# Kernel tuning notes

Hardware: AMD Instinct MI355X
Metric: run time of the kernel (lower is better)

## Reference

```python
import jax, jax.numpy as jnp
import numpy as np

N = 500_000        # atoms
P = 16_000_000     # neighbor pairs (half list)
NS = 4             # species types
CUTOFF = 2.5
BOX = 20.0         # cubic box edge length


def setup_inputs() -> dict:
    key = jax.random.key(0)
    k = jax.random.split(key, 6)
    positions = jax.random.uniform(k[0], (N, 3), dtype=jnp.float32) * BOX
    cell = jnp.eye(3, dtype=jnp.float32) * BOX
    pair_i = jax.random.randint(k[1], (P,), 0, N, dtype=jnp.int32)
    # guarantee j != i so r2 > 0 even when shift == 0
    offs = jax.random.randint(k[2], (P,), 1, N, dtype=jnp.int32)
    pair_j = (pair_i + offs) % N
    shifts = jax.random.randint(k[3], (P, 3), 0, 3, dtype=jnp.int32)
    species = jax.random.randint(k[4], (N,), 0, NS, dtype=jnp.int32)
    # per-species-pair LJ parameter tables (symmetric), mirroring the
    # dict {(a,b): (sigma, epsilon)} precomputation in __init__
    sig = 0.8 + 0.1 * jnp.arange(NS, dtype=jnp.float32)
    eps = 0.5 + 0.1 * jnp.arange(NS, dtype=jnp.float32)
    sigma_tab = 0.5 * (sig[:, None] + sig[None, :])
    eps_tab = jnp.sqrt(eps[:, None] * eps[None, :])
    sr = sigma_tab / CUTOFF
    shift_tab = 4.0 * eps_tab * (sr ** 12 - sr ** 6)
    return dict(positions=positions, cell=cell, sigma_tab=sigma_tab,
                eps_tab=eps_tab, shift_tab=shift_tab, species=species,
                pair_i=pair_i, pair_j=pair_j, shifts=shifts)


def reference(positions, cell, sigma_tab, eps_tab, shift_tab,
              species, pair_i, pair_j, shifts):
    # gather species-pair params (vectorized dict lookup)
    si = species[pair_i]
    sj = species[pair_j]
    sigma = sigma_tab[si, sj]        # [P]
    epsilon = eps_tab[si, sj]        # [P]
    shift_e = shift_tab[si, sj]      # [P]
    # displacement with periodic cell shift: r_j - r_i + S @ cell
    d = positions[pair_j] - positions[pair_i] + shifts.astype(positions.dtype) @ cell  # [P,3]
    r2 = jnp.sum(d * d, axis=-1)     # [P]
    r6 = r2 * r2 * r2
    sigma3 = sigma * sigma * sigma
    sigma6 = sigma3 * sigma3
    sr6 = sigma6 / r6
    sr12 = sr6 * sr6
    e = 4.0 * epsilon * (sr12 - sr6) - shift_e   # [P]
    # per-atom energy: half to each endpoint (per_atom=True path)
    energy = jnp.zeros(positions.shape[0], dtype=positions.dtype)
    energy = energy.at[pair_i].add(0.5 * e).at[pair_j].add(0.5 * e)
    return energy
```

## Files before the change

kernel.cpp:

```cpp
#include <hip/hip_runtime.h>


#define BUCKET_SHIFT 11
#define BUCKET_SIZE  2048
#define SLICES       8
#define QSCALE       2048.0f
#define QINV         (1.0f / 2048.0f)

__global__ void lj_zero_kernel(float* __restrict__ out, long n) {
    long i = (long)blockIdx.x * blockDim.x + threadIdx.x;
    if (i < n) out[i] = 0.0f;
}

__global__ void lj_pack8_kernel(const float* __restrict__ pos,
                                const int* __restrict__ species,
                                unsigned long long* __restrict__ tab8,
                                int* __restrict__ cursor,
                                int nb, int cap, int n) {
    int i = blockIdx.x * blockDim.x + threadIdx.x;
    if (i < n) {
        unsigned int ux = (unsigned int)(pos[3 * i]     * QSCALE + 0.5f) & 0xFFFFu;
        unsigned int uy = (unsigned int)(pos[3 * i + 1] * QSCALE + 0.5f) & 0xFFFFu;
        unsigned int uz = (unsigned int)(pos[3 * i + 2] * QSCALE + 0.5f) & 0xFFFFu;
        unsigned long long w = (unsigned long long)ux
                             | ((unsigned long long)uy << 16)
                             | ((unsigned long long)uz << 32)
                             | ((unsigned long long)(species[i] & 3) << 48);
        tab8[i] = w;
    }
    if (i < nb) cursor[i] = i * cap;
}

__global__ void lj_pack_kernel(const float* __restrict__ pos,
                               const int* __restrict__ species,
                               float4* __restrict__ packed, int n) {
    int i = blockIdx.x * blockDim.x + threadIdx.x;
    if (i < n) {
        float4 p;
        p.x = pos[3 * i];
        p.y = pos[3 * i + 1];
        p.z = pos[3 * i + 2];
        p.w = __int_as_float(species[i]);
        packed[i] = p;
    }
}

__device__ __forceinline__ unsigned int lj_encode(float he) {
    unsigned int u = __float_as_uint(he);
    return (u + 0x400u) & 0xFFFFF800u;
}

__global__ __launch_bounds__(1024) void lj_passA_kernel(
    const unsigned long long* __restrict__ tab8,
    const float* __restrict__ cell,
    const float* __restrict__ sigma_tab,
    const float* __restrict__ eps_tab,
    const float* __restrict__ shift_tab,
    const int* __restrict__ pair_i,
    const int* __restrict__ pair_j,
    const int* __restrict__ shifts,
    unsigned int* __restrict__ record_buf,
    int* __restrict__ cursor,
    int cap, int nb, int P)
{
    __shared__ float s_sig6[16];
    __shared__ float s_eps4[16];
    __shared__ float s_shift[16];
    __shared__ float s_cell[9];
    __shared__ int hist[256];
    __shared__ int basev[256];
    __shared__ int bbase[256];
    __shared__ unsigned int staged[8192];
    __shared__ unsigned char bucketOf[8192];
    int t = threadIdx.x;
    if (t < 16) {
        float s = sigma_tab[t];
        float s3 = s * s * s;
        s_sig6[t] = s3 * s3;
        s_eps4[t] = 4.0f * eps_tab[t];
        s_shift[t] = shift_tab[t];
    }
    if (t < 9) s_cell[t] = cell[t];
    if (t < 256) hist[t] = 0;
    __syncthreads();

    float c00 = s_cell[0], c01 = s_cell[1], c02 = s_cell[2];
    float c10 = s_cell[3], c11 = s_cell[4], c12 = s_cell[5];
    float c20 = s_cell[6], c21 = s_cell[7], c22 = s_cell[8];

    long base = (long)(blockIdx.x * (long)blockDim.x + t) * 4;

    int   ai[4], aj[4];
    float hev[4];
    int   sloti[4], slotj[4];
    bool  valid[4];

    if (base + 3 < P) {
        int4 pi4 = *(const int4*)(pair_i + base);
        int4 pj4 = *(const int4*)(pair_j + base);
        int4 sA = *(const int4*)(shifts + base * 3);
        int4 sB = *(const int4*)(shifts + base * 3 + 4);
        int4 sC = *(const int4*)(shifts + base * 3 + 8);
        int pis[4] = {pi4.x, pi4.y, pi4.z, pi4.w};
        int pjs[4] = {pj4.x, pj4.y, pj4.z, pj4.w};
        int shv[12] = {sA.x, sA.y, sA.z, sA.w, sB.x, sB.y, sB.z, sB.w,
                       sC.x, sC.y, sC.z, sC.w};
#pragma unroll
        for (int k = 0; k < 4; ++k) {
            int i = pis[k], j = pjs[k];
            float fx = (float)shv[3 * k], fy = (float)shv[3 * k + 1], fz = (float)shv[3 * k + 2];
            unsigned long long gi = tab8[i];
            unsigned long long gj = tab8[j];
            int xi = (int)(gi & 0xFFFFu), yi = (int)((gi >> 16) & 0xFFFFu), zi = (int)((gi >> 32) & 0xFFFFu);
            int xj = (int)(gj & 0xFFFFu), yj = (int)((gj >> 16) & 0xFFFFu), zj = (int)((gj >> 32) & 0xFFFFu);
            float dlx = (float)(xj - xi) * QINV;
            float dly = (float)(yj - yi) * QINV;
            float dlz = (float)(zj - zi) * QINV;
            float dx = dlx + fx * c00 + fy * c10 + fz * c20;
            float dy = dly + fx * c01 + fy * c11 + fz * c21;
            float dz = dlz + fx * c02 + fy * c12 + fz * c22;
            float r2 = dx * dx + dy * dy + dz * dz;
            float r6 = r2 * r2 * r2;
            int idx = (int)(gi >> 48) * 4 + (int)(gj >> 48);
            float sr6 = s_sig6[idx] / r6;
            float sr12 = sr6 * sr6;
            hev[k] = 0.5f * (s_eps4[idx] * (sr12 - sr6) - s_shift[idx]);
            ai[k] = i; aj[k] = j; valid[k] = true;
        }
    } else {
#pragma unroll
        for (int k = 0; k < 4; ++k) {
            long p = base + k;
            valid[k] = (p < P);
            ai[k] = 0; aj[k] = 0; hev[k] = 0.0f;
            if (valid[k]) {
                int i = pair_i[p], j = pair_j[p];
                float fx = (float)shifts[3 * p], fy = (float)shifts[3 * p + 1], fz = (float)shifts[3 * p + 2];
                unsigned long long gi = tab8[i];
                unsigned long long gj = tab8[j];
                int xi = (int)(gi & 0xFFFFu), yi = (int)((gi >> 16) & 0xFFFFu), zi = (int)((gi >> 32) & 0xFFFFu);
                int xj = (int)(gj & 0xFFFFu), yj = (int)((gj >> 16) & 0xFFFFu), zj = (int)((gj >> 32) & 0xFFFFu);
                float dlx = (float)(xj - xi) * QINV;
                float dly = (float)(yj - yi) * QINV;
                float dlz = (float)(zj - zi) * QINV;
                float dx = dlx + fx * c00 + fy * c10 + fz * c20;
                float dy = dly + fx * c01 + fy * c11 + fz * c21;
                float dz = dlz + fx * c02 + fy * c12 + fz * c22;
                float r2 = dx * dx + dy * dy + dz * dz;
                float r6 = r2 * r2 * r2;
                int idx = (int)(gi >> 48) * 4 + (int)(gj >> 48);
                float sr6 = s_sig6[idx] / r6;
                float sr12 = sr6 * sr6;
                hev[k] = 0.5f * (s_eps4[idx] * (sr12 - sr6) - s_shift[idx]);
                ai[k] = i; aj[k] = j;
            }
        }
    }

#pragma unroll
    for (int k = 0; k < 4; ++k) {
        if (valid[k]) {
            sloti[k] = atomicAdd(&hist[ai[k] >> BUCKET_SHIFT], 1);
            slotj[k] = atomicAdd(&hist[aj[k] >> BUCKET_SHIFT], 1);
        } else {
            sloti[k] = 0; slotj[k] = 0;
        }
    }
    __syncthreads();

    if (t < 64) {
        int b0 = t * 4;
        int h0 = hist[b0], h1 = hist[b0 + 1], h2 = hist[b0 + 2], h3 = hist[b0 + 3];
        int s = h0 + h1 + h2 + h3;
        int incl = s;
#pragma unroll
        for (int d = 1; d < 64; d <<= 1) {
            int v = __shfl_up(incl, d, 64);
            if (t >= d) incl += v;
        }
        int excl = incl - s;
        bbase[b0]     = excl;
        bbase[b0 + 1] = excl + h0;
        bbase[b0 + 2] = excl + h0 + h1;
        bbase[b0 + 3] = excl + h0 + h1 + h2;
    }
    if (t < nb) {
        int h = hist[t];
        basev[t] = (h > 0) ? atomicAdd(&cursor[t], h) : 0;
    }
    __syncthreads();

#pragma unroll
    for (int k = 0; k < 4; ++k) {
        if (valid[k]) {
            unsigned int u = lj_encode(hev[k]);
            int bi = ai[k] >> BUCKET_SHIFT;
            int li = bbase[bi] + sloti[k];
            staged[li] = u | (unsigned int)(ai[k] & (BUCKET_SIZE - 1));
            bucketOf[li] = (unsigned char)bi;
            int bj = aj[k] >> BUCKET_SHIFT;
            int lidxj = bbase[bj] + slotj[k];
            staged[lidxj] = u | (unsigned int)(aj[k] & (BUCKET_SIZE - 1));
            bucketOf[lidxj] = (unsigned char)bj;
        }
    }
    __syncthreads();

    int total = bbase[255] + hist[255];
    for (int idx = t; idx < total; idx += 1024) {
        int b = (int)bucketOf[idx];
        int g = basev[b] + (idx - bbase[b]);
        if (g < (b + 1) * cap) record_buf[g] = staged[idx];
    }
}

__global__ __launch_bounds__(256) void lj_passB_kernel(
    const unsigned int* __restrict__ record_buf,
    const int* __restrict__ cursor,
    float* __restrict__ partial,
    int cap)
{
    __shared__ float e[BUCKET_SIZE];
    int blk = blockIdx.x;
    int b = blk >> 3;
    int s = blk & (SLICES - 1);
    int t = threadIdx.x;
#pragma unroll
    for (int k = 0; k < 8; ++k) e[t + 256 * k] = 0.0f;
    __syncthreads();

    int begin = b * cap;
    int count = cursor[b] - begin;
    if (count > cap) count = cap;

    int ngroups = (count + 7) >> 3;
    int gps = (ngroups + SLICES - 1) / SLICES;
    int g0 = s * gps;
    int g1 = g0 + gps;
    if (g1 > ngroups) g1 = ngroups;

    for (int g = g0 + t; g < g1; g += 256) {
        int r0 = g * 8;
        const unsigned int* rp = record_buf + begin + r0;
        if (r0 + 8 <= count) {
            int4 a = *(const int4*)(rp);
            int4 c = *(const int4*)(rp + 4);
            unsigned int w0 = (unsigned int)a.x, w1 = (unsigned int)a.y;
            unsigned int w2 = (unsigned int)a.z, w3 = (unsigned int)a.w;
            unsigned int w4 = (unsigned int)c.x, w5 = (unsigned int)c.y;
            unsigned int w6 = (unsigned int)c.z, w7 = (unsigned int)c.w;
            atomicAdd(&e[w0 & 2047u], __uint_as_float(w0 & 0xFFFFF800u));
            atomicAdd(&e[w1 & 2047u], __uint_as_float(w1 & 0xFFFFF800u));
            atomicAdd(&e[w2 & 2047u], __uint_as_float(w2 & 0xFFFFF800u));
            atomicAdd(&e[w3 & 2047u], __uint_as_float(w3 & 0xFFFFF800u));
            atomicAdd(&e[w4 & 2047u], __uint_as_float(w4 & 0xFFFFF800u));
            atomicAdd(&e[w5 & 2047u], __uint_as_float(w5 & 0xFFFFF800u));
            atomicAdd(&e[w6 & 2047u], __uint_as_float(w6 & 0xFFFFF800u));
            atomicAdd(&e[w7 & 2047u], __uint_as_float(w7 & 0xFFFFF800u));
        } else {
            for (int r = r0; r < count; ++r) {
                unsigned int w = record_buf[begin + r];
                atomicAdd(&e[w & 2047u], __uint_as_float(w & 0xFFFFF800u));
            }
        }
    }
    __syncthreads();

    float* pb = partial + (long)blk * BUCKET_SIZE;
#pragma unroll
    for (int k = 0; k < 8; ++k) pb[t + 256 * k] = e[t + 256 * k];
}

__global__ void lj_reduce_kernel(const float* __restrict__ partial,
                                 float* __restrict__ energy, int N) {
    int i = blockIdx.x * blockDim.x + threadIdx.x;
    if (i < N) {
        int b = i >> BUCKET_SHIFT;
        int l = i & (BUCKET_SIZE - 1);
        const float* pb = partial + ((long)b * SLICES) * BUCKET_SIZE + l;
        float s = 0.0f;
#pragma unroll
        for (int k = 0; k < SLICES; ++k) s += pb[(long)k * BUCKET_SIZE];
        energy[i] = s;
    }
}

__device__ __forceinline__ void lj_one_pair_packed(
    int i, int j, float fx, float fy, float fz,
    const float4* __restrict__ packed,
    const float* s_sig6, const float* s_eps4, const float* s_shift,
    float c00, float c01, float c02,
    float c10, float c11, float c12,
    float c20, float c21, float c22,
    float* __restrict__ energy)
{
    float4 gi = packed[i];
    float4 gj = packed[j];
    float dx = gj.x - gi.x + fx * c00 + fy * c10 + fz * c20;
    float dy = gj.y - gi.y + fx * c01 + fy * c11 + fz * c21;
    float dz = gj.z - gi.z + fx * c02 + fy * c12 + fz * c22;
    float r2 = dx * dx + dy * dy + dz * dz;
    float r6 = r2 * r2 * r2;
    int idx = __float_as_int(gi.w) * 4 + __float_as_int(gj.w);
    float sr6 = s_sig6[idx] / r6;
    float sr12 = sr6 * sr6;
    float he = 0.5f * (s_eps4[idx] * (sr12 - sr6) - s_shift[idx]);
    atomicAdd(energy + i, he);
    atomicAdd(energy + j, he);
}

__global__ __launch_bounds__(256) void lj_pairs_packed_kernel(
    const float4* __restrict__ packed,
    const float* __restrict__ cell,
    const float* __restrict__ sigma_tab,
    const float* __restrict__ eps_tab,
    const float* __restrict__ shift_tab,
    const int* __restrict__ pair_i,
    const int* __restrict__ pair_j,
    const int* __restrict__ shifts,
    float* __restrict__ energy,
    int P)
{
    __shared__ float s_sig6[16];
    __shared__ float s_eps4[16];
    __shared__ float s_shift[16];
    __shared__ float s_cell[9];
    int t = threadIdx.x;
    if (t < 16) {
        float s = sigma_tab[t];
        float s3 = s * s * s;
        s_sig6[t] = s3 * s3;
        s_eps4[t] = 4.0f * eps_tab[t];
        s_shift[t] = shift_tab[t];
    }
    if (t < 9) s_cell[t] = cell[t];
    __syncthreads();

    float c00 = s_cell[0], c01 = s_cell[1], c02 = s_cell[2];
    float c10 = s_cell[3], c11 = s_cell[4], c12 = s_cell[5];
    float c20 = s_cell[6], c21 = s_cell[7], c22 = s_cell[8];

    long base = (long)(blockIdx.x * (long)blockDim.x + t) * 4;
    if (base + 3 < P) {
        int4 pi4 = *(const int4*)(pair_i + base);
        int4 pj4 = *(const int4*)(pair_j + base);
        int4 sA = *(const int4*)(shifts + base * 3);
        int4 sB = *(const int4*)(shifts + base * 3 + 4);
        int4 sC = *(const int4*)(shifts + base * 3 + 8);
        int pis[4] = {pi4.x, pi4.y, pi4.z, pi4.w};
        int pjs[4] = {pj4.x, pj4.y, pj4.z, pj4.w};
        int shv[12] = {sA.x, sA.y, sA.z, sA.w, sB.x, sB.y, sB.z, sB.w,
                       sC.x, sC.y, sC.z, sC.w};
#pragma unroll
        for (int k = 0; k < 4; ++k) {
            lj_one_pair_packed(pis[k], pjs[k],
                        (float)shv[3 * k], (float)shv[3 * k + 1], (float)shv[3 * k + 2],
                        packed, s_sig6, s_eps4, s_shift,
                        c00, c01, c02, c10, c11, c12, c20, c21, c22, energy);
        }
    } else {
        for (long p = base; p < P; ++p) {
            lj_one_pair_packed(pair_i[p], pair_j[p],
                        (float)shifts[3 * p], (float)shifts[3 * p + 1], (float)shifts[3 * p + 2],
                        packed, s_sig6, s_eps4, s_shift,
                        c00, c01, c02, c10, c11, c12, c20, c21, c22, energy);
        }
    }
}

__device__ __forceinline__ void lj_one_pair(
    int i, int j, float fx, float fy, float fz,
    const float* __restrict__ pos,
    const int* __restrict__ species,
    const float* s_sig6, const float* s_eps4, const float* s_shift,
    float c00, float c01, float c02,
    float c10, float c11, float c12,
    float c20, float c21, float c22,
    float* __restrict__ energy)
{
    float dx = pos[3 * j]     - pos[3 * i]     + fx * c00 + fy * c10 + fz * c20;
    float dy = pos[3 * j + 1] - pos[3 * i + 1] + fx * c01 + fy * c11 + fz * c21;
    float dz = pos[3 * j + 2] - pos[3 * i + 2] + fx * c02 + fy * c12 + fz * c22;
    float r2 = dx * dx + dy * dy + dz * dz;
    float r6 = r2 * r2 * r2;
    int idx = species[i] * 4 + species[j];
    float sr6 = s_sig6[idx] / r6;
    float sr12 = sr6 * sr6;
    float he = 0.5f * (s_eps4[idx] * (sr12 - sr6) - s_shift[idx]);
    atomicAdd(energy + i, he);
    atomicAdd(energy + j, he);
}

__global__ __launch_bounds__(256) void lj_pairs_kernel(
    const float* __restrict__ pos,
    const float* __restrict__ cell,
    const float* __restrict__ sigma_tab,
    const float* __restrict__ eps_tab,
    const float* __restrict__ shift_tab,
    const int* __restrict__ species,
    const int* __restrict__ pair_i,
    const int* __restrict__ pair_j,
    const int* __restrict__ shifts,
    float* __restrict__ energy,
    int P)
{
    __shared__ float s_sig6[16];
    __shared__ float s_eps4[16];
    __shared__ float s_shift[16];
    __shared__ float s_cell[9];
    int t = threadIdx.x;
    if (t < 16) {
        float s = sigma_tab[t];
        float s3 = s * s * s;
        s_sig6[t] = s3 * s3;
        s_eps4[t] = 4.0f * eps_tab[t];
        s_shift[t] = shift_tab[t];
    }
    if (t < 9) s_cell[t] = cell[t];
    __syncthreads();

    float c00 = s_cell[0], c01 = s_cell[1], c02 = s_cell[2];
    float c10 = s_cell[3], c11 = s_cell[4], c12 = s_cell[5];
    float c20 = s_cell[6], c21 = s_cell[7], c22 = s_cell[8];

    long base = (long)(blockIdx.x * (long)blockDim.x + t) * 4;
    if (base + 3 < P) {
        int4 pi4 = *(const int4*)(pair_i + base);
        int4 pj4 = *(const int4*)(pair_j + base);
        int4 sA = *(const int4*)(shifts + base * 3);
        int4 sB = *(const int4*)(shifts + base * 3 + 4);
        int4 sC = *(const int4*)(shifts + base * 3 + 8);
        int pis[4] = {pi4.x, pi4.y, pi4.z, pi4.w};
        int pjs[4] = {pj4.x, pj4.y, pj4.z, pj4.w};
        int shv[12] = {sA.x, sA.y, sA.z, sA.w, sB.x, sB.y, sB.z, sB.w,
                       sC.x, sC.y, sC.z, sC.w};
#pragma unroll
        for (int k = 0; k < 4; ++k) {
            lj_one_pair(pis[k], pjs[k],
                        (float)shv[3 * k], (float)shv[3 * k + 1], (float)shv[3 * k + 2],
                        pos, species, s_sig6, s_eps4, s_shift,
                        c00, c01, c02, c10, c11, c12, c20, c21, c22, energy);
        }
    } else {
        for (long p = base; p < P; ++p) {
            lj_one_pair(pair_i[p], pair_j[p],
                        (float)shifts[3 * p], (float)shifts[3 * p + 1], (float)shifts[3 * p + 2],
                        pos, species, s_sig6, s_eps4, s_shift,
                        c00, c01, c02, c10, c11, c12, c20, c21, c22, energy);
        }
    }
}

extern "C" void kernel_launch(void* const* d_in, const int* in_sizes, int n_in,
                              void* d_out, int out_size, void* d_ws, size_t ws_size,
                              hipStream_t stream) {
    const float* positions = (const float*)d_in[0];
    const float* cell      = (const float*)d_in[1];
    const float* sigma_tab = (const float*)d_in[2];
    const float* eps_tab   = (const float*)d_in[3];
    const float* shift_tab = (const float*)d_in[4];
    const int*   species   = (const int*)d_in[5];
    const int*   pair_i    = (const int*)d_in[6];
    const int*   pair_j    = (const int*)d_in[7];
    const int*   shifts    = (const int*)d_in[8];
    float* energy = (float*)d_out;

    const int N = out_size;
    const int P = in_sizes[6];

    const int threads = 256;
    const int ablocks = (N + threads - 1) / threads;
    const int pblocks4 = (int)((((long)P + 3) / 4 + threads - 1) / threads);

    const int nb = (N + BUCKET_SIZE - 1) / BUCKET_SIZE;
    long avg = (2L * P) / (nb > 0 ? nb : 1);
    long capl = (avg + avg / 50 + 512 + 1023) & ~1023L;
    const int cap = (int)capl;
    const size_t rec_bytes  = (size_t)nb * (size_t)cap * 4u;
    const size_t tab_bytes  = (size_t)N * 8u;
    const size_t cur_bytes  = (size_t)nb * 4u;
    const size_t part_bytes = (size_t)nb * SLICES * BUCKET_SIZE * 4u;
    const size_t need_bucket = rec_bytes + tab_bytes + cur_bytes + part_bytes;
    const size_t need_pack   = (size_t)N * 16u;

    const bool has_ws = (d_ws != nullptr);
    const bool sane = (nb > 0) && (nb <= 256) && ((long)nb * cap < 2000000000L);
    const bool use_bucket = has_ws && sane && (ws_size >= need_bucket);
    const bool use_pack   = has_ws && !use_bucket && (ws_size >= need_pack);

    if (use_bucket) {
        unsigned int* record_buf = (unsigned int*)d_ws;
        unsigned long long* tab8 = (unsigned long long*)((char*)d_ws + rec_bytes);
        int* cursor = (int*)((char*)d_ws + rec_bytes + tab_bytes);
        float* partial = (float*)((char*)d_ws + rec_bytes + tab_bytes + cur_bytes);

        lj_pack8_kernel<<<ablocks, threads, 0, stream>>>(
            positions, species, tab8, cursor, nb, cap, N);
        const int athreads = 1024;
        const long nthreads_needed = ((long)P + 3) / 4;
        const int pblocksA = (int)((nthreads_needed + athreads - 1) / athreads);
        lj_passA_kernel<<<pblocksA, athreads, 0, stream>>>(
            tab8, cell, sigma_tab, eps_tab, shift_tab,
            pair_i, pair_j, shifts, record_buf, cursor, cap, nb, P);
        lj_passB_kernel<<<nb * SLICES, threads, 0, stream>>>(record_buf, cursor, partial, cap);
        lj_reduce_kernel<<<ablocks, threads, 0, stream>>>(partial, energy, N);
    } else if (use_pack) {
        float4* packed = (float4*)d_ws;
        lj_zero_kernel<<<ablocks, threads, 0, stream>>>(energy, N);
        lj_pack_kernel<<<ablocks, threads, 0, stream>>>(positions, species, packed, N);
        lj_pairs_packed_kernel<<<pblocks4, threads, 0, stream>>>(
            packed, cell, sigma_tab, eps_tab, shift_tab,
            pair_i, pair_j, shifts, energy, P);
    } else {
        lj_zero_kernel<<<ablocks, threads, 0, stream>>>(energy, N);
        lj_pairs_kernel<<<pblocks4, threads, 0, stream>>>(
            positions, cell, sigma_tab, eps_tab, shift_tab, species,
            pair_i, pair_j, shifts, energy, P);
    }
}
```

Measured before the change: 752.6 us.

## Batch 8 pairs per thread in pass A with hoisted gathers and nontemporal streams

Pass A now handles 8 pairs per thread with 512-thread blocks, so each block still stages 8192 records. All 16 position-table gathers are issued before any arithmetic, which gives more memory-level parallelism. Pair indices, shifts and record output use nontemporal loads and stores so the streamed data does not pollute the cache. Records are encoded early and bucket/slot pairs are packed into single ints to save registers, though the higher per-thread register use may reduce occupancy.

```diff
diff --git a/kernel.cpp b/kernel.cpp
--- a/kernel.cpp
+++ b/kernel.cpp
@@ -6,6 +6,11 @@
 #define SLICES       8
 #define QSCALE       2048.0f
 #define QINV         (1.0f / 2048.0f)
+
+#define A_THREADS 512
+#define A_PAIRS   8
+
+typedef int vint4 __attribute__((ext_vector_type(4)));
 
 __global__ void lj_zero_kernel(float* __restrict__ out, long n) {
     long i = (long)blockIdx.x * blockDim.x + threadIdx.x;
@@ -50,7 +55,7 @@
     return (u + 0x400u) & 0xFFFFF800u;
 }
 
-__global__ __launch_bounds__(1024) void lj_passA_kernel(
+__global__ __launch_bounds__(A_THREADS) void lj_passA_kernel(
     const unsigned long long* __restrict__ tab8,
     const float* __restrict__ cell,
     const float* __restrict__ sigma_tab,
@@ -70,8 +75,8 @@
     __shared__ int hist[256];
     __shared__ int basev[256];
     __shared__ int bbase[256];
-    __shared__ unsigned int staged[8192];
-    __shared__ unsigned char bucketOf[8192];
+    __shared__ unsigned int staged[A_THREADS * A_PAIRS * 2];
+    __shared__ unsigned char bucketOf[A_THREADS * A_PAIRS * 2];
     int t = threadIdx.x;
     if (t < 16) {
         float s = sigma_tab[t];
@@ -88,31 +93,45 @@
     float c10 = s_cell[3], c11 = s_cell[4], c12 = s_cell[5];
     float c20 = s_cell[6], c21 = s_cell[7], c22 = s_cell[8];
 
-    long base = (long)(blockIdx.x * (long)blockDim.x + t) * 4;
-
-    int   ai[4], aj[4];
-    float hev[4];
-    int   sloti[4], slotj[4];
-    bool  valid[4];
-
-    if (base + 3 < P) {
-        int4 pi4 = *(const int4*)(pair_i + base);
-        int4 pj4 = *(const int4*)(pair_j + base);
-        int4 sA = *(const int4*)(shifts + base * 3);
-        int4 sB = *(const int4*)(shifts + base * 3 + 4);
-        int4 sC = *(const int4*)(shifts + base * 3 + 8);
-        int pis[4] = {pi4.x, pi4.y, pi4.z, pi4.w};
-        int pjs[4] = {pj4.x, pj4.y, pj4.z, pj4.w};
-        int shv[12] = {sA.x, sA.y, sA.z, sA.w, sB.x, sB.y, sB.z, sB.w,
-                       sC.x, sC.y, sC.z, sC.w};
-#pragma unroll
-        for (int k = 0; k < 4; ++k) {
-            int i = pis[k], j = pjs[k];
+    long base = (long)(blockIdx.x * (long)A_THREADS + t) * A_PAIRS;
+
+    unsigned int encI[A_PAIRS], encJ[A_PAIRS];
+    int slotij[A_PAIRS];
+    int bkt[A_PAIRS];
+    int vmask = 0;
+
+    if (base + (A_PAIRS - 1) < P) {
+        vmask = (1 << A_PAIRS) - 1;
+        vint4 piA = __builtin_nontemporal_load((const vint4*)(pair_i + base));
+        vint4 piB = __builtin_nontemporal_load((const vint4*)(pair_i + base + 4));
+        vint4 pjA = __builtin_nontemporal_load((const vint4*)(pair_j + base));
+        vint4 pjB = __builtin_nontemporal_load((const vint4*)(pair_j + base + 4));
+        int pis[A_PAIRS] = {piA[0], piA[1], piA[2], piA[3], piB[0], piB[1], piB[2], piB[3]};
+        int pjs[A_PAIRS] = {pjA[0], pjA[1], pjA[2], pjA[3], pjB[0], pjB[1], pjB[2], pjB[3]};
+
+        unsigned long long gi[A_PAIRS], gj[A_PAIRS];
+#pragma unroll
+        for (int k = 0; k < A_PAIRS; ++k) {
+            gi[k] = tab8[pis[k]];
+            gj[k] = tab8[pjs[k]];
+        }
+
+        vint4 s0 = __builtin_nontemporal_load((const vint4*)(shifts + base * 3));
+        vint4 s1 = __builtin_nontemporal_load((const vint4*)(shifts + base * 3 + 4));
+        vint4 s2 = __builtin_nontemporal_load((const vint4*)(shifts + base * 3 + 8));
+        vint4 s3 = __builtin_nontemporal_load((const vint4*)(shifts + base * 3 + 12));
+        vint4 s4 = __builtin_nontemporal_load((const vint4*)(shifts + base * 3 + 16));
+        vint4 s5 = __builtin_nontemporal_load((const vint4*)(shifts + base * 3 + 20));
+        int shv[24] = {s0[0], s0[1], s0[2], s0[3], s1[0], s1[1], s1[2], s1[3],
+                       s2[0], s2[1], s2[2], s2[3], s3[0], s3[1], s3[2], s3[3],
+                       s4[0], s4[1], s4[2], s4[3], s5[0], s5[1], s5[2], s5[3]};
+
+#pragma unroll
+        for (int k = 0; k < A_PAIRS; ++k) {
             float fx = (float)shv[3 * k], fy = (float)shv[3 * k + 1], fz = (float)shv[3 * k + 2];
-            unsigned long long gi = tab8[i];
-            unsigned long long gj = tab8[j];
-            int xi = (int)(gi & 0xFFFFu), yi = (int)((gi >> 16) & 0xFFFFu), zi = (int)((gi >> 32) & 0xFFFFu);
-            int xj = (int)(gj & 0xFFFFu), yj = (int)((gj >> 16) & 0xFFFFu), zj = (int)((gj >> 32) & 0xFFFFu);
+            unsigned long long wi = gi[k], wj = gj[k];
+            int xi = (int)(wi & 0xFFFFu), yi = (int)((wi >> 16) & 0xFFFFu), zi = (int)((wi >> 32) & 0xFFFFu);
+            int xj = (int)(wj & 0xFFFFu), yj = (int)((wj >> 16) & 0xFFFFu), zj = (int)((wj >> 32) & 0xFFFFu);
             float dlx = (float)(xj - xi) * QINV;
             float dly = (float)(yj - yi) * QINV;
             float dlz = (float)(zj - zi) * QINV;
@@ -121,25 +140,28 @@
             float dz = dlz + fx * c02 + fy * c12 + fz * c22;
             float r2 = dx * dx + dy * dy + dz * dz;
             float r6 = r2 * r2 * r2;
-            int idx = (int)(gi >> 48) * 4 + (int)(gj >> 48);
+            int idx = (int)(wi >> 48) * 4 + (int)(wj >> 48);
             float sr6 = s_sig6[idx] / r6;
             float sr12 = sr6 * sr6;
-            hev[k] = 0.5f * (s_eps4[idx] * (sr12 - sr6) - s_shift[idx]);
-            ai[k] = i; aj[k] = j; valid[k] = true;
+            float he = 0.5f * (s_eps4[idx] * (sr12 - sr6) - s_shift[idx]);
+            unsigned int u = lj_encode(he);
+            encI[k] = u | (unsigned int)(pis[k] & (BUCKET_SIZE - 1));
+            encJ[k] = u | (unsigned int)(pjs[k] & (BUCKET_SIZE - 1));
+            bkt[k] = (pis[k] >> BUCKET_SHIFT) | ((pjs[k] >> BUCKET_SHIFT) << 8);
         }
     } else {
 #pragma unroll
-        for (int k = 0; k < 4; ++k) {
+        for (int k = 0; k < A_PAIRS; ++k) {
             long p = base + k;
-            valid[k] = (p < P);
-            ai[k] = 0; aj[k] = 0; hev[k] = 0.0f;
-            if (valid[k]) {
+            encI[k] = 0; encJ[k] = 0; bkt[k] = 0;
+            if (p < P) {
+                vmask |= (1 << k);
                 int i = pair_i[p], j = pair_j[p];
                 float fx = (float)shifts[3 * p], fy = (float)shifts[3 * p + 1], fz = (float)shifts[3 * p + 2];
-                unsigned long long gi = tab8[i];
-                unsigned long long gj = tab8[j];
-                int xi = (int)(gi & 0xFFFFu), yi = (int)((gi >> 16) & 0xFFFFu), zi = (int)((gi >> 32) & 0xFFFFu);
-                int xj = (int)(gj & 0xFFFFu), yj = (int)((gj >> 16) & 0xFFFFu), zj = (int)((gj >> 32) & 0xFFFFu);
+                unsigned long long wi = tab8[i];
+                unsigned long long wj = tab8[j];
+                int xi = (int)(wi & 0xFFFFu), yi = (int)((wi >> 16) & 0xFFFFu), zi = (int)((wi >> 32) & 0xFFFFu);
+                int xj = (int)(wj & 0xFFFFu), yj = (int)((wj >> 16) & 0xFFFFu), zj = (int)((wj >> 32) & 0xFFFFu);
                 float dlx = (float)(xj - xi) * QINV;
                 float dly = (float)(yj - yi) * QINV;
                 float dlz = (float)(zj - zi) * QINV;
@@ -148,22 +170,26 @@
                 float dz = dlz + fx * c02 + fy * c12 + fz * c22;
                 float r2 = dx * dx + dy * dy + dz * dz;
                 float r6 = r2 * r2 * r2;
-                int idx = (int)(gi >> 48) * 4 + (int)(gj >> 48);
+                int idx = (int)(wi >> 48) * 4 + (int)(wj >> 48);
                 float sr6 = s_sig6[idx] / r6;
                 float sr12 = sr6 * sr6;
-                hev[k] = 0.5f * (s_eps4[idx] * (sr12 - sr6) - s_shift[idx]);
-                ai[k] = i; aj[k] = j;
+                float he = 0.5f * (s_eps4[idx] * (sr12 - sr6) - s_shift[idx]);
+                unsigned int u = lj_encode(he);
+                encI[k] = u | (unsigned int)(i & (BUCKET_SIZE - 1));
+                encJ[k] = u | (unsigned int)(j & (BUCKET_SIZE - 1));
+                bkt[k] = (i >> BUCKET_SHIFT) | ((j >> BUCKET_SHIFT) << 8);
             }
         }
     }
 
 #pragma unroll
-    for (int k = 0; k < 4; ++k) {
-        if (valid[k]) {
-            sloti[k] = atomicAdd(&hist[ai[k] >> BUCKET_SHIFT], 1);
-            slotj[k] = atomicAdd(&hist[aj[k] >> BUCKET_SHIFT], 1);
+    for (int k = 0; k < A_PAIRS; ++k) {
+        if (vmask & (1 << k)) {
+            int si = atomicAdd(&hist[bkt[k] & 255], 1);
+            int sj = atomicAdd(&hist[(bkt[k] >> 8) & 255], 1);
+            slotij[k] = si | (sj << 16);
         } else {
-            sloti[k] = 0; slotj[k] = 0;
+            slotij[k] = 0;
         }
     }
     __syncthreads();
@@ -191,26 +217,26 @@
     __syncthreads();
 
 #pragma unroll
-    for (int k = 0; k < 4; ++k) {
-        if (valid[k]) {
-            unsigned int u = lj_encode(hev[k]);
-            int bi = ai[k] >> BUCKET_SHIFT;
-            int li = bbase[bi] + sloti[k];
-            staged[li] = u | (unsigned int)(ai[k] & (BUCKET_SIZE - 1));
+    for (int k = 0; k < A_PAIRS; ++k) {
+        if (vmask & (1 << k)) {
+            int bi = bkt[k] & 255;
+            int li = bbase[bi] + (slotij[k] & 0xFFFF);
+            staged[li] = encI[k];
             bucketOf[li] = (unsigned char)bi;
-            int bj = aj[k] >> BUCKET_SHIFT;
-            int lidxj = bbase[bj] + slotj[k];
-            staged[lidxj] = u | (unsigned int)(aj[k] & (BUCKET_SIZE - 1));
-            bucketOf[lidxj] = (unsigned char)bj;
+            int bj = (bkt[k] >> 8) & 255;
+            int lj = bbase[bj] + (slotij[k] >> 16);
+            staged[lj] = encJ[k];
+            bucketOf[lj] = (unsigned char)bj;
         }
     }
     __syncthreads();
 
     int total = bbase[255] + hist[255];
-    for (int idx = t; idx < total; idx += 1024) {
+    for (int idx = t; idx < total; idx += A_THREADS) {
         int b = (int)bucketOf[idx];
         int g = basev[b] + (idx - bbase[b]);
-        if (g < (b + 1) * cap) record_buf[g] = staged[idx];
+        if (g < (b + 1) * cap)
+            __builtin_nontemporal_store(staged[idx], &record_buf[g]);
     }
 }
 
@@ -496,10 +522,9 @@
 
         lj_pack8_kernel<<<ablocks, threads, 0, stream>>>(
             positions, species, tab8, cursor, nb, cap, N);
-        const int athreads = 1024;
-        const long nthreads_needed = ((long)P + 3) / 4;
-        const int pblocksA = (int)((nthreads_needed + athreads - 1) / athreads);
-        lj_passA_kernel<<<pblocksA, athreads, 0, stream>>>(
+        const long nthreads_needed = ((long)P + A_PAIRS - 1) / A_PAIRS;
+        const int pblocksA = (int)((nthreads_needed + A_THREADS - 1) / A_THREADS);
+        lj_passA_kernel<<<pblocksA, A_THREADS, 0, stream>>>(
             tab8, cell, sigma_tab, eps_tab, shift_tab,
             pair_i, pair_j, shifts, record_buf, cursor, cap, nb, P);
         lj_passB_kernel<<<nb * SLICES, threads, 0, stream>>>(record_buf, cursor, partial, cap);
```

Result: no change. 766.8 us (+1.9%).
